# Kernel tuning notes

Hardware: AMD Instinct MI355X
Metric: run time of the kernel (lower is better)

## Reference

```python
import jax, jax.numpy as jnp
import numpy as np

EXPERT_CAPACITY = 320
RMS_EPS = 1e-6


def setup_inputs() -> dict:
    key = jax.random.key(0)
    k1, k2, k3, k4 = jax.random.split(key, 4)
    B, S, D, E, F = 8, 2048, 1024, 8, 2048
    data = jax.random.normal(k1, (B, S, D), dtype=jnp.float32)
    gate_w = jax.random.normal(k2, (D, E), dtype=jnp.float32) * 0.02
    w1 = jax.random.normal(k3, (E, D, F), dtype=jnp.float32) * 0.02
    w2 = jax.random.normal(k4, (E, F, D), dtype=jnp.float32) * 0.02
    rms_w = jnp.ones((D,), dtype=jnp.float32)
    return {"data": data, "gate_w": gate_w, "w1": w1, "w2": w2, "rms_w": rms_w}


def reference(data, gate_w, w1, w2, rms_w):
    B, S, D = data.shape
    E = gate_w.shape[1]
    C = EXPERT_CAPACITY

    # norm_fn: RMSNorm
    var = jnp.mean(data * data, axis=-1, keepdims=True)
    norm = data * jax.lax.rsqrt(var + RMS_EPS) * rms_w  # [B,S,D]

    # route (fp32 gate, no jitter)
    logits = jnp.einsum('bsd,de->bse', norm, gate_w)  # [B,S,E]
    probs = jax.nn.softmax(logits, axis=-1)
    eidx = jnp.argmax(probs, axis=-1)  # [B,S] top-1 expert
    onehot = jax.nn.one_hot(eidx, E, dtype=jnp.int32)  # [B,S,E]
    priority = jnp.cumsum(onehot, axis=1)  # position within expert per batch row
    mask = onehot * (priority <= C)  # capacity-masked dispatch mask [B,S,E]

    pos = jnp.take_along_axis(priority, eidx[..., None], axis=2)[..., 0] - 1  # [B,S]
    kept = jnp.take_along_axis(mask, eidx[..., None], axis=2)[..., 0].astype(bool)
    pos_oob = jnp.where(kept, pos, C)  # OOB -> dropped on scatter

    # dispatch: scatter kept tokens into [B,E,C,D] buffers
    b_idx = jnp.arange(B)[:, None]  # broadcast over S
    buf = jnp.zeros((B, E, C, D), dtype=norm.dtype)
    buf = buf.at[b_idx, eidx, pos_oob].set(norm, mode='drop')

    # per-expert FFN with gelu_new (tanh approx)
    h = jax.nn.gelu(jnp.einsum('becd,edf->becf', buf, w1), approximate=True)
    out_buf = jnp.einsum('becf,efd->becd', h, w2)  # [B,E,C,D]

    # combine: gather expert output; dropped tokens keep norm_data (clone semantics)
    pos_c = jnp.clip(pos_oob, 0, C - 1)
    y = out_buf[b_idx, eidx, pos_c]  # [B,S,D]
    next_states = jnp.where(kept[..., None], y, norm)

    max_prob = jnp.max(probs, axis=-1, keepdims=True)
    hidden = max_prob * next_states
    final = data + hidden  # dropout rate 0

    expert_index_out = jnp.argmax(mask, axis=-1)  # matches torch argmax over masked one-hot
    return final, logits, expert_index_out
```

## Files before the change

### kernel.cpp

```cpp
#include <hip/hip_runtime.h>

typedef __attribute__((ext_vector_type(8))) __bf16 bf16x8;
typedef __attribute__((ext_vector_type(4))) float f32x4;

#define DEVI __device__ __forceinline__

DEVI unsigned short f2bf(float f) {
    unsigned u = __builtin_bit_cast(unsigned, f);
    u += 0x7fffu + ((u >> 16) & 1u);
    return (unsigned short)(u >> 16);
}
DEVI float bf2f(unsigned short h) {
    unsigned u = ((unsigned)h) << 16;
    return __builtin_bit_cast(float, u);
}
DEVI float gelu_tanh(float x) {
    float u = 0.7978845608028654f * (x + 0.044715f * x * x * x);
    float t = 1.0f - 2.0f / (1.0f + __expf(2.0f * u));
    return 0.5f * x * (1.0f + t);
}
DEVI void gload16(const void* g, void* l) {
    __builtin_amdgcn_global_load_lds((const __attribute__((address_space(1))) unsigned int*)g,
                                     (__attribute__((address_space(3))) unsigned int*)l,
                                     16, 0, 0);
}

#define BB 8
#define SS 2048
#define DD 1024
#define EE 8
#define FF 2048
#define CC 320
#define NTOK (BB * SS)
#define MPE (BB * CC)
#define NSLOT (EE * MPE)

__global__ __launch_bounds__(256) void k_rms_gate(
    const float* __restrict__ data, const float* __restrict__ gate_w,
    const float* __restrict__ rms_w, unsigned short* __restrict__ norm_bf,
    float* __restrict__ logits_out, float* __restrict__ maxprob, int* __restrict__ eidx_out)
{
    const int token = blockIdx.x;
    const int t = threadIdx.x;
    const float4 v = ((const float4*)(data + (size_t)token * DD))[t];
    float ss = v.x * v.x + v.y * v.y + v.z * v.z + v.w * v.w;
#pragma unroll
    for (int o = 32; o; o >>= 1) ss += __shfl_down(ss, o, 64);
    __shared__ float sred[4];
    __shared__ float slog[8];
    __shared__ float sacc[4][8];
    if ((t & 63) == 0) sred[t >> 6] = ss;
    __syncthreads();
    const float tot = sred[0] + sred[1] + sred[2] + sred[3];
    const float scale = rsqrtf(tot * (1.0f / 1024.0f) + 1e-6f);
    const float4 w = ((const float4*)rms_w)[t];
    float nn[4] = { v.x * scale * w.x, v.y * scale * w.y, v.z * scale * w.z, v.w * scale * w.w };
    ushort4 nb;
    nb.x = f2bf(nn[0]); nb.y = f2bf(nn[1]); nb.z = f2bf(nn[2]); nb.w = f2bf(nn[3]);
    ((ushort4*)(norm_bf + (size_t)token * DD))[t] = nb;

    float acc[8] = {0, 0, 0, 0, 0, 0, 0, 0};
    const float4* g = (const float4*)(gate_w + t * 32);
#pragma unroll
    for (int d = 0; d < 4; ++d) {
        float4 p = g[2 * d], q = g[2 * d + 1];
        acc[0] += nn[d] * p.x; acc[1] += nn[d] * p.y; acc[2] += nn[d] * p.z; acc[3] += nn[d] * p.w;
        acc[4] += nn[d] * q.x; acc[5] += nn[d] * q.y; acc[6] += nn[d] * q.z; acc[7] += nn[d] * q.w;
    }
#pragma unroll
    for (int e = 0; e < 8; ++e) {
#pragma unroll
        for (int o = 32; o; o >>= 1) acc[e] += __shfl_down(acc[e], o, 64);
    }
    if ((t & 63) == 0) {
#pragma unroll
        for (int e = 0; e < 8; ++e) sacc[t >> 6][e] = acc[e];
    }
    __syncthreads();
    if (t < 8) {
        float l = sacc[0][t] + sacc[1][t] + sacc[2][t] + sacc[3][t];
        logits_out[(size_t)token * 8 + t] = l;
        slog[t] = l;
    }
    __syncthreads();
    if (t == 0) {
        float m = slog[0]; int am = 0;
#pragma unroll
        for (int e = 1; e < 8; ++e) { if (slog[e] > m) { m = slog[e]; am = e; } }
        float s = 0.f;
#pragma unroll
        for (int e = 0; e < 8; ++e) s += __expf(slog[e] - m);
        maxprob[token] = 1.0f / s;
        eidx_out[token] = am;
    }
}

__global__ __launch_bounds__(256) void k_route(
    const int* __restrict__ eidx, int* __restrict__ pos_out,
    float* __restrict__ idxf_out, int* __restrict__ slot_token, int* __restrict__ zp)
{
    const int b = blockIdx.x, t = threadIdx.x;
    if (b == 0) {
        zp[t] = 0; zp[t + 256] = 0;
    }
    for (int i = t; i < EE * CC; i += 256) {
        int e = i / CC, c = i % CC;
        slot_token[e * MPE + b * CC + c] = -1;
    }
    const int base = b * SS + t * 8;
    int e8[8];
#pragma unroll
    for (int j = 0; j < 8; ++j) e8[j] = eidx[base + j];
    int cnt[8] = {0, 0, 0, 0, 0, 0, 0, 0};
#pragma unroll
    for (int j = 0; j < 8; ++j) {
#pragma unroll
        for (int q = 0; q < 8; ++q) cnt[q] += (e8[j] == q);
    }
    __shared__ int sc[8][256];
#pragma unroll
    for (int q = 0; q < 8; ++q) sc[q][t] = cnt[q];
    __syncthreads();
    for (int off = 1; off < 256; off <<= 1) {
        int v[8];
#pragma unroll
        for (int q = 0; q < 8; ++q) v[q] = (t >= off) ? sc[q][t - off] : 0;
        __syncthreads();
#pragma unroll
        for (int q = 0; q < 8; ++q) sc[q][t] += v[q];
        __syncthreads();
    }
    int run[8];
#pragma unroll
    for (int q = 0; q < 8; ++q) run[q] = (t == 0) ? 0 : sc[q][t - 1];
#pragma unroll
    for (int j = 0; j < 8; ++j) {
        const int e = e8[j];
        const int tok = base + j;
        int pos = 0;
#pragma unroll
        for (int q = 0; q < 8; ++q) if (q == e) { pos = run[q]; run[q]++; }
        const bool kept = pos < CC;
        pos_out[tok] = kept ? pos : CC;
        idxf_out[tok] = (float)(kept ? e : 0);
        if (kept) slot_token[e * MPE + b * CC + pos] = tok;
    }
}

DEVI void transcvt_tile(const float* __restrict__ src, unsigned short* __restrict__ dst,
                        int R, int C, int e, int tr, int tc, int t)
{
    __shared__ float tile[32][33];
    const int c = t & 31, r0 = t >> 5;
    const float* s = src + (size_t)e * R * C;
#pragma unroll
    for (int i = 0; i < 4; ++i) {
        int r = r0 + i * 8;
        tile[r][c] = s[(size_t)(tr * 32 + r) * C + tc * 32 + c];
    }
    __syncthreads();
    unsigned short* d = dst + (size_t)e * C * R;
#pragma unroll
    for (int i = 0; i < 4; ++i) {
        int r = r0 + i * 8;
        d[(size_t)(tc * 32 + r) * R + tr * 32 + c] = f2bf(tile[c][r]);
    }
}

__global__ __launch_bounds__(256) void k_transcvt2(
    const float* __restrict__ w1, const float* __restrict__ w2,
    unsigned short* __restrict__ w1T, unsigned short* __restrict__ w2T)
{
    const int bid = blockIdx.x;
    const int t = threadIdx.x;
    if (bid < EE * 32 * 64) {
        const int e = bid / (32 * 64), rem = bid % (32 * 64);
        transcvt_tile(w1, w1T, DD, FF, e, rem / 64, rem % 64, t);
    } else {
        const int b2 = bid - EE * 32 * 64;
        const int e = b2 / (64 * 32), rem = b2 % (64 * 32);
        transcvt_tile(w2, w2T, FF, DD, e, rem / 32, rem % 32, t);
    }
}

template <int MODE>
__global__ __launch_bounds__(256) void k_gemm(
    const unsigned short* __restrict__ A, const unsigned short* __restrict__ Bt,
    unsigned short* __restrict__ H, const int* __restrict__ slot_token,
    const float* __restrict__ maxprob, const float* __restrict__ data,
    float* __restrict__ outF, const unsigned short* __restrict__ zp, int K, int N)
{
    const int ntn = N >> 7;
    const int bid = blockIdx.x;
    const int e = bid & 7;
    const int inner = bid >> 3;
    const int tm = inner / ntn, tn = inner % ntn;

    __shared__ __align__(16) unsigned short sm[17408];
    unsigned short* lsA = sm;
    unsigned short* lsB = sm + 8192;

    const int tid = threadIdx.x;
    const int w = tid >> 6, L = tid & 63;
    const int wr = w >> 1, wc = w & 1;
    const int rr = L & 15, g = L >> 4;
    const int crow = L >> 3, csl = L & 7;
    const int ssl = csl ^ crow;

    const int slot0 = e * MPE + tm * 128;
    const size_t Bbase = ((size_t)e * N + (size_t)tn * 128) * (size_t)K;

    const unsigned short* aptr[4];
    const unsigned short* bptr[4];
#pragma unroll
    for (int ch = 0; ch < 4; ++ch) {
        const int rowl = w * 32 + ch * 8 + crow;
        if (MODE == 0) {
            const int tok = slot_token[slot0 + rowl];
            aptr[ch] = (tok < 0) ? zp : (A + (size_t)tok * DD);
        } else {
            aptr[ch] = A + ((size_t)slot0 + rowl) * (size_t)K;
        }
        bptr[ch] = Bt + Bbase + (size_t)rowl * K;
    }

    f32x4 acc[4][4];
#pragma unroll
    for (int m = 0; m < 4; ++m)
#pragma unroll
        for (int n = 0; n < 4; ++n) acc[m][n] = 0.f;

    const int KT = K >> 6;
    for (int kt = 0; kt < KT; ++kt) {
        const int koff = (kt << 6) + (ssl << 3);
#pragma unroll
        for (int ch = 0; ch < 4; ++ch) {
            gload16(aptr[ch] + koff, lsA + (w * 32 + ch * 8) * 64);
            gload16(bptr[ch] + koff, lsB + (w * 32 + ch * 8) * 64);
        }
        __syncthreads();
#pragma unroll
        for (int ks = 0; ks < 2; ++ks) {
            bf16x8 af[4], bfr[4];
#pragma unroll
            for (int m = 0; m < 4; ++m) {
                const int row = wr * 64 + m * 16 + rr;
                af[m] = *(const bf16x8*)(lsA + row * 64 + ((((ks << 2) | g) ^ (row & 7)) << 3));
            }
#pragma unroll
            for (int n = 0; n < 4; ++n) {
                const int row = wc * 64 + n * 16 + rr;
                bfr[n] = *(const bf16x8*)(lsB + row * 64 + ((((ks << 2) | g) ^ (row & 7)) << 3));
            }
#pragma unroll
            for (int m = 0; m < 4; ++m)
#pragma unroll
                for (int n = 0; n < 4; ++n)
                    acc[m][n] = __builtin_amdgcn_mfma_f32_16x16x32_bf16(af[m], bfr[n], acc[m][n], 0, 0, 0);
        }
        __syncthreads();
    }

    unsigned short* lo = sm;
#pragma unroll
    for (int m = 0; m < 4; ++m)
#pragma unroll
        for (int n = 0; n < 4; ++n) {
            f32x4 a = acc[m][n];
            const int rl = wr * 64 + m * 16 + g * 4;
            const int cl = wc * 64 + n * 16 + rr;
#pragma unroll
            for (int j = 0; j < 4; ++j) {
                float x = a[j];
                if (MODE == 0) x = gelu_tanh(x);
                lo[(rl + j) * 136 + cl] = f2bf(x);
            }
        }
    __syncthreads();

    if (MODE == 0) {
        const size_t hrow0 = (size_t)slot0;
#pragma unroll
        for (int i = 0; i < 8; ++i) {
            const int ch2 = tid + i * 256;
            const int row = ch2 >> 4, off = (ch2 & 15) << 3;
            int4 vv = *(const int4*)(lo + row * 136 + off);
            *(int4*)(H + (hrow0 + row) * 2048 + tn * 128 + off) = vv;
        }
    } else {
#pragma unroll
        for (int i = 0; i < 8; ++i) {
            const int ch2 = tid + i * 256;
            const int row = ch2 >> 4, off = (ch2 & 15) << 3;
            const int tok = slot_token[slot0 + row];
            if (tok < 0) continue;
            const float mp = maxprob[tok];
            int4 yv = *(const int4*)(lo + row * 136 + off);
            const unsigned short* yy = (const unsigned short*)&yv;
            const size_t go = (size_t)tok * DD + (size_t)(tn * 128 + off);
            float4 d0 = *(const float4*)(data + go);
            float4 d1 = *(const float4*)(data + go + 4);
            float4 o0, o1;
            o0.x = d0.x + mp * bf2f(yy[0]);
            o0.y = d0.y + mp * bf2f(yy[1]);
            o0.z = d0.z + mp * bf2f(yy[2]);
            o0.w = d0.w + mp * bf2f(yy[3]);
            o1.x = d1.x + mp * bf2f(yy[4]);
            o1.y = d1.y + mp * bf2f(yy[5]);
            o1.z = d1.z + mp * bf2f(yy[6]);
            o1.w = d1.w + mp * bf2f(yy[7]);
            *(float4*)(outF + go) = o0;
            *(float4*)(outF + go + 4) = o1;
        }
    }
}

__global__ __launch_bounds__(128) void k_fill(
    const int* __restrict__ pos, const float* __restrict__ maxprob,
    const unsigned short* __restrict__ norm_bf, const float* __restrict__ data,
    float* __restrict__ outF)
{
    const int tok = blockIdx.x;
    if (pos[tok] < CC) return;
    const float mp = maxprob[tok];
    const int t = threadIdx.x;
    const size_t o = (size_t)tok * DD + (size_t)t * 8;
    float4 d0 = *(const float4*)(data + o);
    float4 d1 = *(const float4*)(data + o + 4);
    ushort4 n0 = *(const ushort4*)(norm_bf + o);
    ushort4 n1 = *(const ushort4*)(norm_bf + o + 4);
    float4 r0, r1;
    r0.x = d0.x + mp * bf2f(n0.x);
    r0.y = d0.y + mp * bf2f(n0.y);
    r0.z = d0.z + mp * bf2f(n0.z);
    r0.w = d0.w + mp * bf2f(n0.w);
    r1.x = d1.x + mp * bf2f(n1.x);
    r1.y = d1.y + mp * bf2f(n1.y);
    r1.z = d1.z + mp * bf2f(n1.z);
    r1.w = d1.w + mp * bf2f(n1.w);
    *(float4*)(outF + o) = r0;
    *(float4*)(outF + o + 4) = r1;
}

extern "C" void kernel_launch(void* const* d_in, const int* in_sizes, int n_in,
                              void* d_out, int out_size, void* d_ws, size_t ws_size,
                              hipStream_t stream)
{
    (void)in_sizes; (void)n_in; (void)out_size; (void)ws_size;
    const float* data   = (const float*)d_in[0];
    const float* gate_w = (const float*)d_in[1];
    const float* w1     = (const float*)d_in[2];
    const float* w2     = (const float*)d_in[3];
    const float* rms_w  = (const float*)d_in[4];

    float* outF   = (float*)d_out;
    float* logits = outF + (size_t)NTOK * DD;
    float* idxf   = logits + (size_t)NTOK * EE;

    char* ws = (char*)d_ws;
    const size_t SZ_NORM = (size_t)NTOK * DD * 2;
    const size_t SZ_W1T  = (size_t)EE * DD * FF * 2;
    const size_t SZ_W2T  = SZ_W1T;
    const size_t SZ_H    = (size_t)NSLOT * FF * 2;
    unsigned short* norm_bf = (unsigned short*)(ws);
    unsigned short* w1T     = (unsigned short*)(ws + SZ_NORM);
    unsigned short* w2T     = (unsigned short*)(ws + SZ_NORM + SZ_W1T);
    unsigned short* Hbuf    = (unsigned short*)(ws + SZ_NORM + SZ_W1T + SZ_W2T);
    char* small             = ws + SZ_NORM + SZ_W1T + SZ_W2T + SZ_H;
    int*   slot_token = (int*)(small);
    int*   pos        = (int*)(small + NSLOT * 4);
    int*   eidx       = (int*)(small + NSLOT * 4 + NTOK * 4);
    float* maxprob    = (float*)(small + NSLOT * 4 + NTOK * 4 + NTOK * 4);
    int*   zp         = (int*)(small + NSLOT * 4 + NTOK * 4 + NTOK * 4 + NTOK * 4);

    k_rms_gate<<<NTOK, 256, 0, stream>>>(data, gate_w, rms_w, norm_bf, logits, maxprob, eidx);
    k_route<<<BB, 256, 0, stream>>>(eidx, pos, idxf, slot_token, zp);
    k_transcvt2<<<EE * 32 * 64 * 2, 256, 0, stream>>>(w1, w2, w1T, w2T);
    k_gemm<0><<<EE * 20 * (FF / 128), 256, 0, stream>>>(norm_bf, w1T, Hbuf, slot_token, nullptr, nullptr, nullptr, (const unsigned short*)zp, DD, FF);
    k_gemm<1><<<EE * 20 * (DD / 128), 256, 0, stream>>>(Hbuf, w2T, nullptr, slot_token, maxprob, data, outF, nullptr, FF, DD);
    k_fill<<<NTOK, 128, 0, stream>>>(pos, maxprob, norm_bf, data, outF);
}
```

Baseline: 522.0 us.

## Replace expert GEMMs with 256x256 pipelined 8-wave kernel and fuse fill

The expert FFN GEMMs move from 128x128 tiles with 4 waves to 256x256 tiles with 8 waves. They use a double-buffered 128KB LDS ping-pong schedule with global_load_lds prefetch, phase barriers and s_setprio around the MFMA blocks. The dropped-token fill kernel is removed: the RMS/gate kernel now writes data + maxprob*norm for every token, and the GEMM epilogue overwrites the kept tokens. The weight transpose-convert uses 64x64 tiles with vectorized loads and stores. The larger tiles cut redundant operand loads and overlap copy with compute, at the cost of fewer blocks (640 and 320), which may underfill the GPU, and an extra full-output write.

```diff
diff --git a/kernel.cpp b/kernel.cpp
--- a/kernel.cpp
+++ b/kernel.cpp
@@ -38,7 +38,8 @@
 __global__ __launch_bounds__(256) void k_rms_gate(
     const float* __restrict__ data, const float* __restrict__ gate_w,
     const float* __restrict__ rms_w, unsigned short* __restrict__ norm_bf,
-    float* __restrict__ logits_out, float* __restrict__ maxprob, int* __restrict__ eidx_out)
+    float* __restrict__ logits_out, float* __restrict__ maxprob, int* __restrict__ eidx_out,
+    float* __restrict__ outF)
 {
     const int token = blockIdx.x;
     const int t = threadIdx.x;
@@ -49,6 +50,7 @@
     __shared__ float sred[4];
     __shared__ float slog[8];
     __shared__ float sacc[4][8];
+    __shared__ float smp;
     if ((t & 63) == 0) sred[t >> 6] = ss;
     __syncthreads();
     const float tot = sred[0] + sred[1] + sred[2] + sred[3];
@@ -90,19 +92,25 @@
         float s = 0.f;
 #pragma unroll
         for (int e = 0; e < 8; ++e) s += __expf(slog[e] - m);
-        maxprob[token] = 1.0f / s;
+        const float mp = 1.0f / s;
+        maxprob[token] = mp;
+        smp = mp;
         eidx_out[token] = am;
     }
+    __syncthreads();
+    const float mp = smp;
+    float4 o;
+    o.x = v.x + mp * nn[0]; o.y = v.y + mp * nn[1];
+    o.z = v.z + mp * nn[2]; o.w = v.w + mp * nn[3];
+    ((float4*)(outF + (size_t)token * DD))[t] = o;
 }
 
 __global__ __launch_bounds__(256) void k_route(
-    const int* __restrict__ eidx, int* __restrict__ pos_out,
-    float* __restrict__ idxf_out, int* __restrict__ slot_token, int* __restrict__ zp)
+    const int* __restrict__ eidx, float* __restrict__ idxf_out,
+    int* __restrict__ slot_token, int* __restrict__ zp)
 {
     const int b = blockIdx.x, t = threadIdx.x;
-    if (b == 0) {
-        zp[t] = 0; zp[t + 256] = 0;
-    }
+    if (b == 0) { zp[t] = 0; zp[t + 256] = 0; zp[t + 512] = 0; zp[t + 768] = 0; }
     for (int i = t; i < EE * CC; i += 256) {
         int e = i / CC, c = i % CC;
         slot_token[e * MPE + b * CC + c] = -1;
@@ -141,205 +149,214 @@
 #pragma unroll
         for (int q = 0; q < 8; ++q) if (q == e) { pos = run[q]; run[q]++; }
         const bool kept = pos < CC;
-        pos_out[tok] = kept ? pos : CC;
         idxf_out[tok] = (float)(kept ? e : 0);
         if (kept) slot_token[e * MPE + b * CC + pos] = tok;
     }
 }
 
-DEVI void transcvt_tile(const float* __restrict__ src, unsigned short* __restrict__ dst,
-                        int R, int C, int e, int tr, int tc, int t)
-{
-    __shared__ float tile[32][33];
-    const int c = t & 31, r0 = t >> 5;
-    const float* s = src + (size_t)e * R * C;
-#pragma unroll
-    for (int i = 0; i < 4; ++i) {
-        int r = r0 + i * 8;
-        tile[r][c] = s[(size_t)(tr * 32 + r) * C + tc * 32 + c];
-    }
-    __syncthreads();
-    unsigned short* d = dst + (size_t)e * C * R;
-#pragma unroll
-    for (int i = 0; i < 4; ++i) {
-        int r = r0 + i * 8;
-        d[(size_t)(tc * 32 + r) * R + tr * 32 + c] = f2bf(tile[c][r]);
-    }
-}
-
-__global__ __launch_bounds__(256) void k_transcvt2(
+__global__ __launch_bounds__(256) void k_transcvt3(
     const float* __restrict__ w1, const float* __restrict__ w2,
     unsigned short* __restrict__ w1T, unsigned short* __restrict__ w2T)
 {
-    const int bid = blockIdx.x;
-    const int t = threadIdx.x;
-    if (bid < EE * 32 * 64) {
-        const int e = bid / (32 * 64), rem = bid % (32 * 64);
-        transcvt_tile(w1, w1T, DD, FF, e, rem / 64, rem % 64, t);
+    __shared__ float tile[64][68];
+    const int bid = blockIdx.x, t = threadIdx.x;
+    const float* src; unsigned short* dst; int C, R, tr, tc;
+    if (bid < 4096) {
+        const int e = bid >> 9, rem = bid & 511;
+        tr = rem >> 5; tc = rem & 31;
+        src = w1 + (size_t)e * (DD * FF); dst = w1T + (size_t)e * (DD * FF);
+        R = DD; C = FF;
     } else {
-        const int b2 = bid - EE * 32 * 64;
-        const int e = b2 / (64 * 32), rem = b2 % (64 * 32);
-        transcvt_tile(w2, w2T, FF, DD, e, rem / 32, rem % 32, t);
-    }
-}
-
-template <int MODE>
-__global__ __launch_bounds__(256) void k_gemm(
-    const unsigned short* __restrict__ A, const unsigned short* __restrict__ Bt,
+        const int b2 = bid - 4096;
+        const int e = b2 >> 9, rem = b2 & 511;
+        tr = rem >> 4; tc = rem & 15;
+        src = w2 + (size_t)e * (DD * FF); dst = w2T + (size_t)e * (DD * FF);
+        R = FF; C = DD;
+    }
+    const int r = t >> 2, c0 = (t & 3) << 4;
+    const float4* sp = (const float4*)(src + (size_t)(tr * 64 + r) * C + tc * 64 + c0);
+#pragma unroll
+    for (int i = 0; i < 4; ++i) *(float4*)&tile[r][c0 + 4 * i] = sp[i];
+    __syncthreads();
+    const int oc = t >> 2, i0 = (t & 3) << 4;
+    union { unsigned short us[16]; int4 q[2]; } u;
+#pragma unroll
+    for (int i = 0; i < 16; ++i) u.us[i] = f2bf(tile[i0 + i][oc]);
+    unsigned short* dp = dst + (size_t)(tc * 64 + oc) * R + tr * 64 + i0;
+    *(int4*)dp = u.q[0];
+    *(int4*)(dp + 8) = u.q[1];
+}
+
+#define LD_A(buf, h) { _Pragma("unroll") for (int mp_ = 0; mp_ < 4; ++mp_) { \
+    const int lr_ = mp_ * 16 + rr; \
+    _Pragma("unroll") for (int ks_ = 0; ks_ < 2; ++ks_) \
+      ar_[mp_][ks_] = *(const bf16x8*)(sm + (buf) * 65536 + (h) * 16384 + wm * 8192 + lr_ * 128 + ((ks_ * 64 + g * 16) ^ (((lr_ >> 2) & 1) << 5))); } }
+
+#define LD_B(buf, h, reg) { _Pragma("unroll") for (int np_ = 0; np_ < 2; ++np_) { \
+    const int lr_ = np_ * 16 + rr; \
+    _Pragma("unroll") for (int ks_ = 0; ks_ < 2; ++ks_) \
+      reg[np_][ks_] = *(const bf16x8*)(sm + (buf) * 65536 + 32768 + (h) * 16384 + wn * 4096 + lr_ * 128 + ((ks_ * 64 + g * 16) ^ (((lr_ >> 2) & 1) << 5))); } }
+
+#define MM(qa, qb, reg) { _Pragma("unroll") for (int ks_ = 0; ks_ < 2; ++ks_) \
+    _Pragma("unroll") for (int mp_ = 0; mp_ < 4; ++mp_) \
+    _Pragma("unroll") for (int np_ = 0; np_ < 2; ++np_) \
+      acc[(qa) * 4 + mp_][(qb) * 2 + np_] = __builtin_amdgcn_mfma_f32_16x16x32_bf16(ar_[mp_][ks_], reg[np_][ks_], acc[(qa) * 4 + mp_][(qb) * 2 + np_], 0, 0, 0); }
+
+#define ST_A(buf, h, kt) { \
+    gload16(srcA[h][0] + (kt) * 64, sm + (buf) * 65536 + (h) * 16384 + tid * 16); \
+    gload16(srcA[h][1] + (kt) * 64, sm + (buf) * 65536 + (h) * 16384 + 8192 + tid * 16); }
+#define ST_B(buf, h, kt) { \
+    gload16(srcB[h][0] + (kt) * 64, sm + (buf) * 65536 + 32768 + (h) * 16384 + tid * 16); \
+    gload16(srcB[h][1] + (kt) * 64, sm + (buf) * 65536 + 32768 + (h) * 16384 + 8192 + tid * 16); }
+
+#define PH_TOP  __builtin_amdgcn_s_barrier(); \
+                asm volatile("s_waitcnt lgkmcnt(0)" ::: "memory"); \
+                __builtin_amdgcn_s_setprio(1)
+#define PH_END  __builtin_amdgcn_s_setprio(0); __builtin_amdgcn_s_barrier()
+#define PH_END_VM4 __builtin_amdgcn_s_setprio(0); \
+                asm volatile("s_waitcnt vmcnt(4)" ::: "memory"); __builtin_amdgcn_s_barrier()
+#define PH_END_VM0 __builtin_amdgcn_s_setprio(0); \
+                asm volatile("s_waitcnt vmcnt(0)" ::: "memory"); __builtin_amdgcn_s_barrier()
+
+template <int MODE, int K, int NT_N>
+__global__ __launch_bounds__(512) void k_gemm8(
+    const unsigned short* __restrict__ Ap, const unsigned short* __restrict__ Bt,
     unsigned short* __restrict__ H, const int* __restrict__ slot_token,
     const float* __restrict__ maxprob, const float* __restrict__ data,
-    float* __restrict__ outF, const unsigned short* __restrict__ zp, int K, int N)
-{
-    const int ntn = N >> 7;
+    float* __restrict__ outF, const unsigned short* __restrict__ zp)
+{
+    __shared__ __align__(16) unsigned char sm[131072];
     const int bid = blockIdx.x;
     const int e = bid & 7;
     const int inner = bid >> 3;
-    const int tm = inner / ntn, tn = inner % ntn;
-
-    __shared__ __align__(16) unsigned short sm[17408];
-    unsigned short* lsA = sm;
-    unsigned short* lsB = sm + 8192;
-
+    const int tm = inner / NT_N, tn = inner % NT_N;
     const int tid = threadIdx.x;
-    const int w = tid >> 6, L = tid & 63;
-    const int wr = w >> 1, wc = w & 1;
+    const int L = tid & 63;
+    const int wm = tid >> 8;
+    const int wn = (tid >> 6) & 3;
     const int rr = L & 15, g = L >> 4;
-    const int crow = L >> 3, csl = L & 7;
-    const int ssl = csl ^ crow;
-
-    const int slot0 = e * MPE + tm * 128;
-    const size_t Bbase = ((size_t)e * N + (size_t)tn * 128) * (size_t)K;
-
-    const unsigned short* aptr[4];
-    const unsigned short* bptr[4];
-#pragma unroll
-    for (int ch = 0; ch < 4; ++ch) {
-        const int rowl = w * 32 + ch * 8 + crow;
+    const int slot0 = e * MPE + tm * 256;
+    const int N = NT_N * 256;
+
+    const unsigned short* srcA[2][2];
+    const unsigned short* srcB[2][2];
+#pragma unroll
+    for (int h = 0; h < 2; ++h)
+#pragma unroll
+      for (int p = 0; p < 2; ++p) {
+        const int o = p * 8192 + tid * 16;
+        const int lo = o ^ (((o >> 9) & 1) << 5);
+        const int cb = lo & 127;
+        const int arr = (lo >> 7) & 63;
+        const int arow = p * 128 + h * 64 + arr;
         if (MODE == 0) {
-            const int tok = slot_token[slot0 + rowl];
-            aptr[ch] = (tok < 0) ? zp : (A + (size_t)tok * DD);
+            const int tok = slot_token[slot0 + arow];
+            srcA[h][p] = (tok < 0 ? zp : Ap + (size_t)tok * (size_t)K) + (cb >> 1);
         } else {
-            aptr[ch] = A + ((size_t)slot0 + rowl) * (size_t)K;
+            srcA[h][p] = Ap + (size_t)(slot0 + arow) * (size_t)K + (cb >> 1);
         }
-        bptr[ch] = Bt + Bbase + (size_t)rowl * K;
-    }
-
-    f32x4 acc[4][4];
-#pragma unroll
-    for (int m = 0; m < 4; ++m)
-#pragma unroll
-        for (int n = 0; n < 4; ++n) acc[m][n] = 0.f;
-
-    const int KT = K >> 6;
-    for (int kt = 0; kt < KT; ++kt) {
-        const int koff = (kt << 6) + (ssl << 3);
-#pragma unroll
-        for (int ch = 0; ch < 4; ++ch) {
-            gload16(aptr[ch] + koff, lsA + (w * 32 + ch * 8) * 64);
-            gload16(bptr[ch] + koff, lsB + (w * 32 + ch * 8) * 64);
+        const int bwn = o >> 12;
+        const int brr = (lo >> 7) & 31;
+        const int nrow = tn * 256 + bwn * 64 + h * 32 + brr;
+        srcB[h][p] = Bt + ((size_t)e * N + nrow) * (size_t)K + (cb >> 1);
+    }
+
+    f32x4 acc[8][4];
+#pragma unroll
+    for (int m = 0; m < 8; ++m)
+#pragma unroll
+      for (int n = 0; n < 4; ++n) acc[m][n] = 0.f;
+    bf16x8 ar_[4][2], br0_[2][2], br1_[2][2];
+
+    ST_A(0, 0, 0); ST_B(0, 0, 0); ST_A(0, 1, 0); ST_B(0, 1, 0);
+    ST_A(1, 0, 1); ST_B(1, 1, 1);
+    asm volatile("s_waitcnt vmcnt(4)" ::: "memory");
+    __builtin_amdgcn_s_barrier();
+
+    const int NT = K / 64;
+    const int NITER = NT / 2;
+    for (int it = 0; it < NITER - 1; ++it) {
+        const int t1 = 2 * it + 1;
+        LD_A(0, 0); LD_B(0, 0, br0_); ST_A(1, 1, t1);
+        PH_TOP; MM(0, 0, br0_); PH_END;
+        LD_B(0, 1, br1_); ST_B(1, 0, t1);
+        PH_TOP; MM(0, 1, br1_); PH_END;
+        LD_A(0, 1); ST_A(0, 0, t1 + 1);
+        PH_TOP; MM(1, 1, br1_); PH_END;
+        ST_B(0, 1, t1 + 1);
+        PH_TOP; MM(1, 0, br0_); PH_END_VM4;
+        LD_A(1, 0); LD_B(1, 0, br0_); ST_A(0, 1, t1 + 1);
+        PH_TOP; MM(0, 0, br0_); PH_END;
+        LD_B(1, 1, br1_); ST_B(0, 0, t1 + 1);
+        PH_TOP; MM(0, 1, br1_); PH_END;
+        LD_A(1, 1); ST_A(1, 0, t1 + 2);
+        PH_TOP; MM(1, 1, br1_); PH_END;
+        ST_B(1, 1, t1 + 2);
+        PH_TOP; MM(1, 0, br0_); PH_END_VM4;
+    }
+    {
+        LD_A(0, 0); LD_B(0, 0, br0_); ST_A(1, 1, NT - 1);
+        PH_TOP; MM(0, 0, br0_); PH_END;
+        LD_B(0, 1, br1_); ST_B(1, 0, NT - 1);
+        PH_TOP; MM(0, 1, br1_); PH_END;
+        LD_A(0, 1);
+        PH_TOP; MM(1, 1, br1_); PH_END;
+        PH_TOP; MM(1, 0, br0_); PH_END_VM0;
+        LD_A(1, 0); LD_B(1, 0, br0_);
+        PH_TOP; MM(0, 0, br0_); PH_END;
+        LD_B(1, 1, br1_);
+        PH_TOP; MM(0, 1, br1_); PH_END;
+        LD_A(1, 1);
+        PH_TOP; MM(1, 1, br1_); PH_END;
+        PH_TOP; MM(1, 0, br0_); PH_END;
+    }
+
+    unsigned short* lo16 = (unsigned short*)sm;
+#pragma unroll
+    for (int hb = 0; hb < 2; ++hb) {
+        if (wm == hb) {
+#pragma unroll
+            for (int m = 0; m < 8; ++m)
+#pragma unroll
+              for (int n = 0; n < 4; ++n) {
+                f32x4 a = acc[m][n];
+#pragma unroll
+                for (int j = 0; j < 4; ++j) {
+                    float x = a[j];
+                    if (MODE == 0) x = gelu_tanh(x);
+                    lo16[(m * 16 + g * 4 + j) * 260 + wn * 64 + n * 16 + rr] = f2bf(x);
+                }
+              }
         }
         __syncthreads();
 #pragma unroll
-        for (int ks = 0; ks < 2; ++ks) {
-            bf16x8 af[4], bfr[4];
-#pragma unroll
-            for (int m = 0; m < 4; ++m) {
-                const int row = wr * 64 + m * 16 + rr;
-                af[m] = *(const bf16x8*)(lsA + row * 64 + ((((ks << 2) | g) ^ (row & 7)) << 3));
+        for (int rd = 0; rd < 8; ++rd) {
+            const int idx = rd * 512 + tid;
+            const int row = idx >> 5, c8 = (idx & 31) << 3;
+            if (MODE == 0) {
+                int4 v = *(const int4*)(lo16 + row * 260 + c8);
+                *(int4*)(H + (size_t)(slot0 + hb * 128 + row) * FF + (size_t)tn * 256 + c8) = v;
+            } else {
+                const int tok = slot_token[slot0 + hb * 128 + row];
+                if (tok >= 0) {
+                    const float mp = maxprob[tok];
+                    int4 yv = *(const int4*)(lo16 + row * 260 + c8);
+                    const unsigned short* yy = (const unsigned short*)&yv;
+                    const size_t go = (size_t)tok * DD + (size_t)tn * 256 + c8;
+                    float4 d0 = *(const float4*)(data + go);
+                    float4 d1 = *(const float4*)(data + go + 4);
+                    float4 o0, o1;
+                    o0.x = d0.x + mp * bf2f(yy[0]); o0.y = d0.y + mp * bf2f(yy[1]);
+                    o0.z = d0.z + mp * bf2f(yy[2]); o0.w = d0.w + mp * bf2f(yy[3]);
+                    o1.x = d1.x + mp * bf2f(yy[4]); o1.y = d1.y + mp * bf2f(yy[5]);
+                    o1.z = d1.z + mp * bf2f(yy[6]); o1.w = d1.w + mp * bf2f(yy[7]);
+                    *(float4*)(outF + go) = o0;
+                    *(float4*)(outF + go + 4) = o1;
+                }
             }
-#pragma unroll
-            for (int n = 0; n < 4; ++n) {
-                const int row = wc * 64 + n * 16 + rr;
-                bfr[n] = *(const bf16x8*)(lsB + row * 64 + ((((ks << 2) | g) ^ (row & 7)) << 3));
-            }
-#pragma unroll
-            for (int m = 0; m < 4; ++m)
-#pragma unroll
-                for (int n = 0; n < 4; ++n)
-                    acc[m][n] = __builtin_amdgcn_mfma_f32_16x16x32_bf16(af[m], bfr[n], acc[m][n], 0, 0, 0);
         }
         __syncthreads();
     }
-
-    unsigned short* lo = sm;
-#pragma unroll
-    for (int m = 0; m < 4; ++m)
-#pragma unroll
-        for (int n = 0; n < 4; ++n) {
-            f32x4 a = acc[m][n];
-            const int rl = wr * 64 + m * 16 + g * 4;
-            const int cl = wc * 64 + n * 16 + rr;
-#pragma unroll
-            for (int j = 0; j < 4; ++j) {
-                float x = a[j];
-                if (MODE == 0) x = gelu_tanh(x);
-                lo[(rl + j) * 136 + cl] = f2bf(x);
-            }
-        }
-    __syncthreads();
-
-    if (MODE == 0) {
-        const size_t hrow0 = (size_t)slot0;
-#pragma unroll
-        for (int i = 0; i < 8; ++i) {
-            const int ch2 = tid + i * 256;
-            const int row = ch2 >> 4, off = (ch2 & 15) << 3;
-            int4 vv = *(const int4*)(lo + row * 136 + off);
-            *(int4*)(H + (hrow0 + row) * 2048 + tn * 128 + off) = vv;
-        }
-    } else {
-#pragma unroll
-        for (int i = 0; i < 8; ++i) {
-            const int ch2 = tid + i * 256;
-            const int row = ch2 >> 4, off = (ch2 & 15) << 3;
-            const int tok = slot_token[slot0 + row];
-            if (tok < 0) continue;
-            const float mp = maxprob[tok];
-            int4 yv = *(const int4*)(lo + row * 136 + off);
-            const unsigned short* yy = (const unsigned short*)&yv;
-            const size_t go = (size_t)tok * DD + (size_t)(tn * 128 + off);
-            float4 d0 = *(const float4*)(data + go);
-            float4 d1 = *(const float4*)(data + go + 4);
-            float4 o0, o1;
-            o0.x = d0.x + mp * bf2f(yy[0]);
-            o0.y = d0.y + mp * bf2f(yy[1]);
-            o0.z = d0.z + mp * bf2f(yy[2]);
-            o0.w = d0.w + mp * bf2f(yy[3]);
-            o1.x = d1.x + mp * bf2f(yy[4]);
-            o1.y = d1.y + mp * bf2f(yy[5]);
-            o1.z = d1.z + mp * bf2f(yy[6]);
-            o1.w = d1.w + mp * bf2f(yy[7]);
-            *(float4*)(outF + go) = o0;
-            *(float4*)(outF + go + 4) = o1;
-        }
-    }
-}
-
-__global__ __launch_bounds__(128) void k_fill(
-    const int* __restrict__ pos, const float* __restrict__ maxprob,
-    const unsigned short* __restrict__ norm_bf, const float* __restrict__ data,
-    float* __restrict__ outF)
-{
-    const int tok = blockIdx.x;
-    if (pos[tok] < CC) return;
-    const float mp = maxprob[tok];
-    const int t = threadIdx.x;
-    const size_t o = (size_t)tok * DD + (size_t)t * 8;
-    float4 d0 = *(const float4*)(data + o);
-    float4 d1 = *(const float4*)(data + o + 4);
-    ushort4 n0 = *(const ushort4*)(norm_bf + o);
-    ushort4 n1 = *(const ushort4*)(norm_bf + o + 4);
-    float4 r0, r1;
-    r0.x = d0.x + mp * bf2f(n0.x);
-    r0.y = d0.y + mp * bf2f(n0.y);
-    r0.z = d0.z + mp * bf2f(n0.z);
-    r0.w = d0.w + mp * bf2f(n0.w);
-    r1.x = d1.x + mp * bf2f(n1.x);
-    r1.y = d1.y + mp * bf2f(n1.y);
-    r1.z = d1.z + mp * bf2f(n1.z);
-    r1.w = d1.w + mp * bf2f(n1.w);
-    *(float4*)(outF + o) = r0;
-    *(float4*)(outF + o + 4) = r1;
 }
 
 extern "C" void kernel_launch(void* const* d_in, const int* in_sizes, int n_in,
@@ -368,15 +385,15 @@
     unsigned short* Hbuf    = (unsigned short*)(ws + SZ_NORM + SZ_W1T + SZ_W2T);
     char* small             = ws + SZ_NORM + SZ_W1T + SZ_W2T + SZ_H;
     int*   slot_token = (int*)(small);
-    int*   pos        = (int*)(small + NSLOT * 4);
-    int*   eidx       = (int*)(small + NSLOT * 4 + NTOK * 4);
-    float* maxprob    = (float*)(small + NSLOT * 4 + NTOK * 4 + NTOK * 4);
-    int*   zp         = (int*)(small + NSLOT * 4 + NTOK * 4 + NTOK * 4 + NTOK * 4);
-
-    k_rms_gate<<<NTOK, 256, 0, stream>>>(data, gate_w, rms_w, norm_bf, logits, maxprob, eidx);
-    k_route<<<BB, 256, 0, stream>>>(eidx, pos, idxf, slot_token, zp);
-    k_transcvt2<<<EE * 32 * 64 * 2, 256, 0, stream>>>(w1, w2, w1T, w2T);
-    k_gemm<0><<<EE * 20 * (FF / 128), 256, 0, stream>>>(norm_bf, w1T, Hbuf, slot_token, nullptr, nullptr, nullptr, (const unsigned short*)zp, DD, FF);
-    k_gemm<1><<<EE * 20 * (DD / 128), 256, 0, stream>>>(Hbuf, w2T, nullptr, slot_token, maxprob, data, outF, nullptr, FF, DD);
-    k_fill<<<NTOK, 128, 0, stream>>>(pos, maxprob, norm_bf, data, outF);
-}
+    int*   eidx       = (int*)(small + NSLOT * 4);
+    float* maxprob    = (float*)(small + NSLOT * 4 + NTOK * 4);
+    int*   zp         = (int*)(small + NSLOT * 4 + NTOK * 4 + NTOK * 4);
+
+    k_rms_gate<<<NTOK, 256, 0, stream>>>(data, gate_w, rms_w, norm_bf, logits, maxprob, eidx, outF);
+    k_route<<<BB, 256, 0, stream>>>(eidx, idxf, slot_token, zp);
+    k_transcvt3<<<8192, 256, 0, stream>>>(w1, w2, w1T, w2T);
+    k_gemm8<0, 1024, 8><<<640, 512, 0, stream>>>(norm_bf, w1T, Hbuf, slot_token,
+                                                 nullptr, nullptr, nullptr, (const unsigned short*)zp);
+    k_gemm8<1, 2048, 4><<<320, 512, 0, stream>>>(Hbuf, w2T, nullptr, slot_token,
+                                                 maxprob, data, outF, nullptr);
+}
```

Result: slower. 565.4 us (+8.3%).
